# Performance work log

Measured on AMD Instinct MI355X. Metric: run time of the kernel, lower is better.

The kernel has to match this reference:

```python
import jax, jax.numpy as jnp
import numpy as np

B, L, D = 2, 2048, 2048
H, HKV, HD = 16, 4, 128
GROUPS = H // HKV


def _rope_tables(key):
    # standard RoPE cos/sin tables, shape (B, L, HD)
    inv_freq = 1.0 / (10000.0 ** (jnp.arange(0, HD, 2, dtype=jnp.float32) / HD))
    pos = jnp.arange(L, dtype=jnp.float32)
    freqs = pos[:, None] * inv_freq[None, :]          # (L, HD/2)
    emb = jnp.concatenate([freqs, freqs], axis=-1)    # (L, HD)
    cos = jnp.broadcast_to(jnp.cos(emb)[None], (B, L, HD))
    sin = jnp.broadcast_to(jnp.sin(emb)[None], (B, L, HD))
    return cos, sin


def setup_inputs() -> dict:
    key = jax.random.key(0)
    ks = jax.random.split(key, 5)
    x = jax.random.normal(ks[0], (B, L, D), dtype=jnp.float32)
    cos, sin = _rope_tables(ks[1])
    s = 1.0 / np.sqrt(D)
    Wq = jax.random.normal(ks[2], (D, D), dtype=jnp.float32) * s
    bq = jnp.zeros((D,), dtype=jnp.float32)
    Wkv = jax.random.normal(ks[3], (2 * HKV * HD, D), dtype=jnp.float32) * s
    bkv = jnp.zeros((2 * HKV * HD,), dtype=jnp.float32)
    Wo = jax.random.normal(ks[4], (D, D), dtype=jnp.float32) * s
    bo = jnp.zeros((D,), dtype=jnp.float32)
    return {"x": x, "cos": cos, "sin": sin, "Wq": Wq, "bq": bq,
            "Wkv": Wkv, "bkv": bkv, "Wo": Wo, "bo": bo}


def _rotate_half(t):
    t1, t2 = jnp.split(t, 2, axis=-1)
    return jnp.concatenate([-t2, t1], axis=-1)


def reference(x, cos, sin, Wq, bq, Wkv, bkv, Wo, bo):
    b, l, d = x.shape
    # QKV projections
    q = (x @ Wq.T + bq).reshape(b, l, H, HD)
    kv = (x @ Wkv.T + bkv).reshape(b, l, 2, HKV, HD)
    k, v = kv[:, :, 0], kv[:, :, 1]
    # RoPE (unsqueeze over head dim, layout B,L,H,D)
    c = cos[:, :, None, :]
    s = sin[:, :, None, :]
    q = q * c + _rotate_half(q) * s
    k = k * c + _rotate_half(k) * s
    # GQA: expand kv heads to query heads
    k = jnp.repeat(k, GROUPS, axis=2)
    v = jnp.repeat(v, GROUPS, axis=2)
    # causal attention (flash_attn_func equivalent math)
    scores = jnp.einsum("blhd,bmhd->bhlm", q, k) / jnp.sqrt(jnp.float32(HD))
    mask = jnp.tril(jnp.ones((l, l), dtype=bool))
    scores = jnp.where(mask[None, None], scores, jnp.finfo(scores.dtype).min)
    attn = jax.nn.softmax(scores, axis=-1)
    out = jnp.einsum("bhlm,bmhd->blhd", attn, v).reshape(b, l, H * HD)
    return out @ Wo.T + bo
```

## Files before the change

kernel.cpp:

```cpp
#include <hip/hip_runtime.h>
#include <hip/hip_bf16.h>
#include <cstddef>

constexpr int B = 2, L = 2048, D = 2048;
constexpr int H = 16, HKV = 4, HD = 128;
constexpr int GROUPS = H / HKV;
constexpr int KVD = 2 * HKV * HD;
constexpr int M_ROWS = B * L;
constexpr int QKVW = D + KVD;

typedef __attribute__((ext_vector_type(8))) short short8;
typedef __attribute__((ext_vector_type(4))) short s16x4;
typedef __attribute__((ext_vector_type(4))) float f32x4;

__device__ __forceinline__ short f2bf(float f) {
    union { float f; unsigned u; } v; v.f = f;
    unsigned r = v.u + 0x7FFFu + ((v.u >> 16) & 1u);
    return (short)(r >> 16);
}

__device__ __forceinline__ float fast_exp2(float x) {
#if __has_builtin(__builtin_amdgcn_exp2f)
    return __builtin_amdgcn_exp2f(x);
#else
    return exp2f(x);
#endif
}

__device__ __forceinline__ int invp(int pos) {
    const int b16 = pos >> 4, j = pos & 15;
    return ((b16 >> 1) << 4) + j + ((b16 & 1) << 6);
}

typedef __attribute__((address_space(1))) const void cg_void;
typedef __attribute__((address_space(3))) void lds_void;
__device__ __forceinline__ void gl_lds16(const void* g, void* l) {
    __builtin_amdgcn_global_load_lds((cg_void*)g, (lds_void*)l, 16, 0, 0);
}

__global__ __launch_bounds__(256) void cast_all(
    const float* __restrict__ x, const float* __restrict__ Wq,
    const float* __restrict__ Wkv, const float* __restrict__ Wo,
    const float* __restrict__ bq, const float* __restrict__ bkv,
    short* __restrict__ xb, short* __restrict__ wqkvb, short* __restrict__ wob,
    float* __restrict__ bqkv)
{
    constexpr int n_x   = M_ROWS * D / 4;
    constexpr int n_wq  = D * D / 4;
    constexpr int n_wkv = KVD * D / 4;
    constexpr int n_wo  = D * D / 4;
    constexpr int n_w   = n_x + n_wq + n_wkv + n_wo;
    constexpr int RPW   = D / 4;
    int i = blockIdx.x * 256 + threadIdx.x;
    if (i >= n_w) {
        const int j = i - n_w;
        float4 o;
#pragma unroll
        for (int e = 0; e < 4; ++e) {
            const int idx = j * 4 + e;
            float v;
            if (idx < D)                 v = bq[((idx >> 7) << 7) + invp(idx & 127)];
            else if (idx < D + HKV * HD) v = bkv[(((idx - D) >> 7) << 7) + invp((idx - D) & 127)];
            else                         v = bkv[idx - D];
            (&o.x)[e] = v;
        }
        ((float4*)bqkv)[j] = o;
        return;
    }
    const float* src; short* dst; int isrc;
    if (i < n_x) {
        src = x; dst = xb; isrc = i;
    } else if (i < n_x + n_wq) {
        i -= n_x; src = Wq; dst = wqkvb;
        const int fi = i / RPW, col = i % RPW;
        const int head = fi >> 7, pos = fi & 127;
        isrc = ((head << 7) + invp(pos)) * RPW + col;
    } else if (i < n_x + n_wq + n_wkv) {
        i -= n_x + n_wq; src = Wkv; dst = wqkvb + (size_t)D * D;
        const int fi = i / RPW, col = i % RPW;
        if (fi < HKV * HD) {
            isrc = (((fi >> 7) << 7) + invp(fi & 127)) * RPW + col;
        } else {
            isrc = i;
        }
    } else {
        i -= n_x + n_wq + n_wkv; src = Wo; dst = wob; isrc = i;
    }
    const float4 f = ((const float4*)src)[isrc];
    s16x4 s;
    s[0] = f2bf(f.x); s[1] = f2bf(f.y); s[2] = f2bf(f.z); s[3] = f2bf(f.w);
    ((s16x4*)dst)[i] = s;
}

template<int MODE>
__global__ __launch_bounds__(512, 2) void gemm256(
    const short* __restrict__ Ag, const short* __restrict__ Wg,
    const float* __restrict__ bias, float* __restrict__ C,
    const float* __restrict__ cosp, const float* __restrict__ sinp,
    short* __restrict__ qout, short* __restrict__ kout, short* __restrict__ vtout,
    int M, int N, int K)
{
    __shared__ __align__(1024) char smem[131072];

    const int tid = threadIdx.x;
    const int w = tid >> 6, lane = tid & 63;
    const int quad = lane >> 4, n16 = lane & 15;
    const int wr = w >> 2, wc = w & 3;

    const int nbx = gridDim.x;
    const int nwg = nbx * gridDim.y;
    int wg = blockIdx.y * nbx + blockIdx.x;
    wg = (wg & 7) * (nwg >> 3) + (wg >> 3);
    const int bm = (wg / nbx) << 8;
    const int bn = (wg % nbx) << 8;

    const int nkt = K >> 6;

    const int sbo = n16 * 64 + ((quad * 16) ^ ((n16 & 8) << 2));

    const int srow = lane >> 2;
    const int scol = ((lane & 3) * 8) ^ (((lane >> 5) & 1) << 4);

    f32x4 acc[8][4];
#pragma unroll
    for (int i = 0; i < 8; ++i)
#pragma unroll
        for (int j = 0; j < 4; ++j)
#pragma unroll
            for (int r = 0; r < 4; ++r) acc[i][j][r] = 0.f;

    short8 afr[4][2], bfr[4][2];

#define STAGE_A(k0, cb, h)                                                     \
    { _Pragma("unroll") for (int j = 0; j < 2; ++j) {                          \
        const int s  = w + j * 8;                                              \
        const int u  = s >> 1;                                                 \
        const int rg = ((u >> 2) << 3) + ((h) << 2) + (u & 3);                 \
        const int gr = bm + (rg << 4) + srow;                                  \
        const int gc = (k0) + ((s & 1) << 5) + scol;                           \
        gl_lds16(Ag + (size_t)gr * K + gc,                                     \
                 smem + (cb) * 32768 + (h) * 16384 + (s << 10)); } }

#define STAGE_B(k0, cb, h)                                                     \
    { _Pragma("unroll") for (int j = 0; j < 2; ++j) {                          \
        const int s  = w + j * 8;                                              \
        const int u  = s >> 1;                                                 \
        const int rg = ((u >> 1) << 2) + ((h) << 1) + (u & 1);                 \
        const int gr = bn + (rg << 4) + srow;                                  \
        const int gc = (k0) + ((s & 1) << 5) + scol;                           \
        gl_lds16(Wg + (size_t)gr * K + gc,                                     \
                 smem + 65536 + (cb) * 32768 + (h) * 16384 + (s << 10)); } }

#define PHASE(CB, MH, RDB, STAGE_STMT, WAIT_STMT)                              \
    {                                                                          \
        if (RDB) {                                                             \
            _Pragma("unroll") for (int nj = 0; nj < 4; ++nj)                   \
            _Pragma("unroll") for (int kk = 0; kk < 2; ++kk)                   \
                bfr[nj][kk] = *(const short8*)(smem + 65536 + (CB) * 32768 +   \
                    (nj >> 1) * 16384 +                                        \
                    ((((wc * 2 + (nj & 1)) * 2) + kk) << 10) + sbo);           \
        }                                                                      \
        _Pragma("unroll") for (int mi2 = 0; mi2 < 4; ++mi2)                    \
        _Pragma("unroll") for (int kk = 0; kk < 2; ++kk)                       \
            afr[mi2][kk] = *(const short8*)(smem + (CB) * 32768 +              \
                (MH) * 16384 + ((((wr * 4 + mi2) * 2) + kk) << 10) + sbo);     \
        STAGE_STMT;                                                            \
        WAIT_STMT;                                                             \
        __builtin_amdgcn_s_barrier();                                          \
        asm volatile("s_waitcnt lgkmcnt(0)" ::: "memory");                     \
        __builtin_amdgcn_sched_barrier(0);                                     \
        __builtin_amdgcn_s_setprio(1);                                         \
        _Pragma("unroll") for (int mi2 = 0; mi2 < 4; ++mi2)                    \
        _Pragma("unroll") for (int nj = 0; nj < 4; ++nj)                       \
        _Pragma("unroll") for (int kk = 0; kk < 2; ++kk)                       \
            acc[(MH) * 4 + mi2][nj] =                                          \
                __builtin_amdgcn_mfma_f32_16x16x32_bf16(                       \
                    afr[mi2][kk], bfr[nj][kk], acc[(MH) * 4 + mi2][nj],        \
                    0, 0, 0);                                                  \
        __builtin_amdgcn_s_setprio(0);                                         \
        asm volatile("" ::: "memory");                                         \
        __builtin_amdgcn_s_barrier();                                          \
    }

#define NOP_WAIT asm volatile("" ::: "memory")

    STAGE_A(0, 0, 0);
    STAGE_B(0, 0, 0);
    STAGE_A(0, 0, 1);
    STAGE_B(0, 0, 1);
    if (nkt > 1) {
        STAGE_A(64, 1, 0);
        STAGE_B(64, 1, 0);
        asm volatile("s_waitcnt vmcnt(4)" ::: "memory");
    } else {
        asm volatile("s_waitcnt vmcnt(0)" ::: "memory");
    }
    __builtin_amdgcn_s_barrier();

    for (int t = 0; t < nkt; t += 2) {
        const int k1 = (t + 1) << 6, k2 = (t + 2) << 6, k3 = (t + 3) << 6;
        const bool g2 = (t + 2) < nkt, g3 = (t + 3) < nkt;

        PHASE(0, 0, 1, { STAGE_A(k1, 1, 1); STAGE_B(k1, 1, 1); }, NOP_WAIT);
        PHASE(0, 1, 0, { if (g2) { STAGE_A(k2, 0, 0); STAGE_B(k2, 0, 0); } },
              { if (g2) asm volatile("s_waitcnt vmcnt(4)" ::: "memory");
                else    asm volatile("s_waitcnt vmcnt(0)" ::: "memory"); });

        PHASE(1, 0, 1, { if (g2) { STAGE_A(k2, 0, 1); STAGE_B(k2, 0, 1); } }, NOP_WAIT);
        PHASE(1, 1, 0, { if (g3) { STAGE_A(k3, 1, 0); STAGE_B(k3, 1, 0); } },
              { if (g3) asm volatile("s_waitcnt vmcnt(4)" ::: "memory");
                else    asm volatile("s_waitcnt vmcnt(0)" ::: "memory"); });
    }

#undef PHASE
#undef STAGE_A
#undef STAGE_B
#undef NOP_WAIT

    if (MODE == 0) {
#pragma unroll
        for (int mh = 0; mh < 2; ++mh)
#pragma unroll
            for (int mi2 = 0; mi2 < 4; ++mi2)
#pragma unroll
                for (int r = 0; r < 4; ++r) {
                    const int row = bm + wr * 128 + mh * 64 + mi2 * 16 + quad * 4 + r;
#pragma unroll
                    for (int nh = 0; nh < 2; ++nh)
#pragma unroll
                        for (int ni2 = 0; ni2 < 2; ++ni2) {
                            const int col = bn + wc * 64 + nh * 32 + ni2 * 16 + n16;
                            C[(size_t)row * N + col] =
                                acc[mh * 4 + mi2][nh * 2 + ni2][r] + bias[col];
                        }
                }
    } else {
        short* const T = (short*)smem;
        __syncthreads();
        if (bn < D + HKV * HD) {
#pragma unroll
            for (int mh = 0; mh < 2; ++mh)
#pragma unroll
                for (int mi2 = 0; mi2 < 4; ++mi2)
#pragma unroll
                    for (int r = 0; r < 4; ++r) {
                        const int rl = wr * 128 + mh * 64 + mi2 * 16 + quad * 4 + r;
                        const int row = bm + rl;
                        const float* csrow = cosp + (size_t)row * HD;
                        const float* snrow = sinp + (size_t)row * HD;
                        const int sw = ((rl >> 2) & 7) << 4;
#pragma unroll
                        for (int nh = 0; nh < 2; ++nh) {
                            const int cl = wc * 64 + nh * 32 + n16;
                            const int iif = (wc & 1) * 32 + nh * 16 + n16;
                            const float a  = acc[mh * 4 + mi2][nh * 2 + 0][r] + bias[bn + cl];
                            const float bb = acc[mh * 4 + mi2][nh * 2 + 1][r] + bias[bn + cl + 16];
                            const float olo = a * csrow[iif]       - bb * snrow[iif];
                            const float ohi = bb * csrow[iif + 64] + a * snrow[iif + 64];
                            *(short*)((char*)T + ((rl * 512 + cl * 2) ^ sw))        = f2bf(olo);
                            *(short*)((char*)T + ((rl * 512 + (cl + 16) * 2) ^ sw)) = f2bf(ohi);
                        }
                    }
            __syncthreads();
            const bool isK = (bn >= D);
#pragma unroll
            for (int it = 0; it < 16; ++it) {
                const int idx = it * 512 + tid;
                const int rl = idx >> 5, c8 = idx & 31;
                const short8 v = *(const short8*)((char*)T +
                    ((rl * 512 + c8 * 16) ^ (((rl >> 2) & 7) << 4)));
                const int row = bm + rl;
                if (!isK) {
                    *(short8*)&qout[(size_t)row * D + bn + c8 * 8] = v;
                } else {
                    const int ck = bn - D + c8 * 8;
                    const int hk = ck >> 7, dk = ck & 127;
                    const int b_ = row >> 11, l_ = row & (L - 1);
                    *(short8*)&kout[((size_t)(b_ * HKV + hk) * L + l_) * HD + dk] = v;
                }
            }
        } else {
#pragma unroll
            for (int mh = 0; mh < 2; ++mh)
#pragma unroll
                for (int mi2 = 0; mi2 < 4; ++mi2) {
                    const int l0 = wr * 128 + mh * 64 + mi2 * 16 + quad * 4;
#pragma unroll
                    for (int nh = 0; nh < 2; ++nh)
#pragma unroll
                        for (int ni2 = 0; ni2 < 2; ++ni2) {
                            const int cl = wc * 64 + nh * 32 + ni2 * 16 + n16;
                            const float bs = bias[bn + cl];
                            s16x4 sv;
#pragma unroll
                            for (int r = 0; r < 4; ++r)
                                sv[r] = f2bf(acc[mh * 4 + mi2][nh * 2 + ni2][r] + bs);
                            *(s16x4*)((char*)T + ((cl * 512 + l0 * 2) ^ ((cl & 7) << 4))) = sv;
                        }
                }
            __syncthreads();
#pragma unroll
            for (int it = 0; it < 16; ++it) {
                const int idx = it * 512 + tid;
                const int cvr = idx >> 5, l8 = idx & 31;
                const short8 v = *(const short8*)((char*)T +
                    ((cvr * 512 + l8 * 16) ^ ((cvr & 7) << 4)));
                const int cv = bn - (D + HKV * HD) + cvr;
                const int hv = cv >> 7, dv = cv & 127;
                const int b_ = bm >> 11;
                const int lg = (bm & (L - 1)) + l8 * 8;
                *(short8*)&vtout[((size_t)(b_ * HKV + hv) * HD + dv) * L + lg] = v;
            }
        }
    }
}

__global__ __launch_bounds__(512, 2) void gemm_out(
    const short* __restrict__ Ag, const short* __restrict__ Wg,
    const float* __restrict__ bias, float* __restrict__ C,
    int M, int N, int K)
{
    __shared__ __align__(1024) char smem[98304];

    const int tid = threadIdx.x;
    const int w = tid >> 6, lane = tid & 63;
    const int quad = lane >> 4, n16 = lane & 15;
    const int wr = w >> 2, wc = w & 3;

    const int nbx = gridDim.x;
    const int nwg = nbx * gridDim.y;
    int wg = blockIdx.y * nbx + blockIdx.x;
    wg = (wg & 7) * (nwg >> 3) + (wg >> 3);
    const int bm = (wg / nbx) << 7;
    const int bn = (wg % nbx) << 8;

    const int nkt = K >> 6;

    const int sbo = n16 * 64 + ((quad * 16) ^ ((n16 & 8) << 2));
    const int srow = lane >> 2;
    const int scol = ((lane & 3) * 8) ^ (((lane >> 5) & 1) << 4);

    f32x4 acc[4][4];
#pragma unroll
    for (int i = 0; i < 4; ++i)
#pragma unroll
        for (int j = 0; j < 4; ++j)
#pragma unroll
            for (int r = 0; r < 4; ++r) acc[i][j][r] = 0.f;

    short8 afr[4], bfr[4];

#define OSTAGE_A(k0, cb, kh)                                                   \
    { const int gr = bm + (w << 4) + srow;                                     \
      const int gc = (k0) + ((kh) << 5) + scol;                                \
      gl_lds16(Ag + (size_t)gr * K + gc,                                       \
               smem + (cb) * 16384 + (kh) * 8192 + (w << 10)); }

#define OSTAGE_B(k0, cb, kh)                                                   \
    { _Pragma("unroll") for (int j = 0; j < 2; ++j) {                          \
        const int s = w + j * 8;                                               \
        const int gr = bn + (s << 4) + srow;                                   \
        const int gc = (k0) + ((kh) << 5) + scol;                              \
        gl_lds16(Wg + (size_t)gr * K + gc,                                     \
                 smem + 32768 + (cb) * 32768 + (kh) * 16384 + (s << 10)); } }

#define OPHASE(CB, KH, STAGE_STMT, WAIT_STMT)                                  \
    {                                                                          \
        _Pragma("unroll") for (int mi = 0; mi < 4; ++mi)                       \
            afr[mi] = *(const short8*)(smem + (CB) * 16384 + (KH) * 8192 +     \
                ((wr * 4 + mi) << 10) + sbo);                                  \
        _Pragma("unroll") for (int nj = 0; nj < 4; ++nj)                       \
            bfr[nj] = *(const short8*)(smem + 32768 + (CB) * 32768 +           \
                (KH) * 16384 + ((wc * 4 + nj) << 10) + sbo);                   \
        STAGE_STMT;                                                            \
        WAIT_STMT;                                                             \
        __builtin_amdgcn_s_barrier();                                          \
        asm volatile("s_waitcnt lgkmcnt(0)" ::: "memory");                     \
        __builtin_amdgcn_sched_barrier(0);                                     \
        __builtin_amdgcn_s_setprio(1);                                         \
        _Pragma("unroll") for (int mi = 0; mi < 4; ++mi)                       \
        _Pragma("unroll") for (int nj = 0; nj < 4; ++nj)                       \
            acc[mi][nj] = __builtin_amdgcn_mfma_f32_16x16x32_bf16(             \
                afr[mi], bfr[nj], acc[mi][nj], 0, 0, 0);                       \
        __builtin_amdgcn_s_setprio(0);                                         \
        asm volatile("" ::: "memory");                                         \
        __builtin_amdgcn_s_barrier();                                          \
    }

#define ONOP asm volatile("" ::: "memory")

    OSTAGE_A(0, 0, 0);
    OSTAGE_B(0, 0, 0);
    OSTAGE_A(0, 0, 1);
    OSTAGE_B(0, 0, 1);
    if (nkt > 1) {
        OSTAGE_A(64, 1, 0);
        OSTAGE_B(64, 1, 0);
        asm volatile("s_waitcnt vmcnt(3)" ::: "memory");
    } else {
        asm volatile("s_waitcnt vmcnt(0)" ::: "memory");
    }
    __builtin_amdgcn_s_barrier();

    for (int t = 0; t < nkt; t += 2) {
        const int k1 = (t + 1) << 6, k2 = (t + 2) << 6, k3 = (t + 3) << 6;
        const bool g2 = (t + 2) < nkt, g3 = (t + 3) < nkt;

        OPHASE(0, 0, { OSTAGE_A(k1, 1, 1); OSTAGE_B(k1, 1, 1); }, ONOP);
        OPHASE(0, 1, { if (g2) { OSTAGE_A(k2, 0, 0); OSTAGE_B(k2, 0, 0); } },
               { if (g2) asm volatile("s_waitcnt vmcnt(3)" ::: "memory");
                 else    asm volatile("s_waitcnt vmcnt(0)" ::: "memory"); });

        OPHASE(1, 0, { if (g2) { OSTAGE_A(k2, 0, 1); OSTAGE_B(k2, 0, 1); } }, ONOP);
        OPHASE(1, 1, { if (g3) { OSTAGE_A(k3, 1, 0); OSTAGE_B(k3, 1, 0); } },
               { if (g3) asm volatile("s_waitcnt vmcnt(3)" ::: "memory");
                 else    asm volatile("s_waitcnt vmcnt(0)" ::: "memory"); });
    }

#undef OPHASE
#undef OSTAGE_A
#undef OSTAGE_B
#undef ONOP

#pragma unroll
    for (int mi = 0; mi < 4; ++mi)
#pragma unroll
        for (int r = 0; r < 4; ++r) {
            const int row = bm + wr * 64 + mi * 16 + quad * 4 + r;
#pragma unroll
            for (int nj = 0; nj < 4; ++nj) {
                const int col = bn + wc * 64 + nj * 16 + n16;
                C[(size_t)row * N + col] = acc[mi][nj][r] + bias[col];
            }
        }
}

__global__ __launch_bounds__(512, 4) void attn_mfma5(
    const short* __restrict__ qb_, const short* __restrict__ kb_,
    const short* __restrict__ vtb_, short* __restrict__ ob)
{
    __shared__ __align__(16) char smem[75776];
    short* const KsB  = (short*)smem;
    short* const VtB  = (short*)(smem + 32768);
    short* const PbB  = (short*)(smem + 65536);
    float* const Rbuf = (float*)smem;

    const int hkv = blockIdx.y, b = blockIdx.z;
    const int tid = threadIdx.x;
    const int w = tid >> 6, lane = tid & 63;
    const int quad = lane >> 4, n16 = lane & 15;
    const int h   = hkv * GROUPS + (w & 3);
    const int kh  = (w >> 2) * 32;
    const int khg = (w >> 2) * 4;

    const size_t kbase  = (size_t)(b * HKV + hkv) * L * HD;
    const size_t vtbase = (size_t)(b * HKV + hkv) * HD * L;
    const float c1 = 0.12751845f;
    const float c0 = -28.853901f;

    short8 ones;
#pragma unroll
    for (int i = 0; i < 8; ++i) ones[i] = (short)0x3F80;

    const int kr = lane >> 4;
    const int kg_sw = lane & 15;
    const int vr = lane >> 3;
    const int vg_sw = lane & 7;

    short* const myPb = PbB + w * (16 * 40);

#pragma unroll 1
    for (int phase = 0; phase < 2; ++phase) {
        const int qidx = phase ? (127 - (int)blockIdx.x) : (int)blockIdx.x;
        const int qb0 = qidx * 16;
        const int ntiles = (qidx >> 2) + 1;

        short8 qf[4];
#pragma unroll
        for (int kk = 0; kk < 4; ++kk)
            qf[kk] = *(const short8*)&qb_[
                ((size_t)(b * L + qb0 + n16)) * D + h * HD + kk * 32 + quad * 8];

        f32x4 oacc[8], lacc;
#pragma unroll
        for (int r = 0; r < 4; ++r) lacc[r] = 0.f;
#pragma unroll
        for (int nt = 0; nt < 8; ++nt)
#pragma unroll
            for (int r = 0; r < 4; ++r) oacc[nt][r] = 0.f;

        __syncthreads();

        {
            const short* kg = kb_ + kbase;
            const short* vg = vtb_ + vtbase;
#pragma unroll
            for (int j = 0; j < 2; ++j) {
                const int chunk = w * 2 + j;
                const int r = chunk * 4 + kr;
                gl_lds16(kg + r * HD + (kg_sw ^ (r & 15)) * 8, KsB + chunk * 512);
            }
#pragma unroll
            for (int j = 0; j < 2; ++j) {
                const int chunk = w * 2 + j;
                const int d = chunk * 8 + vr;
                gl_lds16(vg + (size_t)d * L + (vg_sw ^ (d & 7)) * 8, VtB + chunk * 512);
            }
        }

        for (int kt = 0; kt < ntiles; ++kt) {
            const int buf = kt & 1;
            __syncthreads();

            if (kt + 1 < ntiles) {
                const short* kg = kb_ + kbase + (size_t)((kt + 1) * 64) * HD;
                const short* vg = vtb_ + vtbase + (kt + 1) * 64;
#pragma unroll
                for (int j = 0; j < 2; ++j) {
                    const int chunk = w * 2 + j;
                    const int r = chunk * 4 + kr;
                    gl_lds16(kg + r * HD + (kg_sw ^ (r & 15)) * 8,
                             KsB + (buf ^ 1) * 8192 + chunk * 512);
                }
#pragma unroll
                for (int j = 0; j < 2; ++j) {
                    const int chunk = w * 2 + j;
                    const int d = chunk * 8 + vr;
                    gl_lds16(vg + (size_t)d * L + (vg_sw ^ (d & 7)) * 8,
                             VtB + (buf ^ 1) * 8192 + chunk * 512);
                }
            }

            const short* Ks = KsB + buf * 8192;
            const short* Vt = VtB + buf * 8192;

            f32x4 s[2];
#pragma unroll
            for (int ktl = 0; ktl < 2; ++ktl)
#pragma unroll
                for (int r = 0; r < 4; ++r) s[ktl][r] = 0.f;
            __builtin_amdgcn_s_setprio(1);
#pragma unroll
            for (int kk = 0; kk < 4; ++kk) {
                short8 kf[2];
#pragma unroll
                for (int ktl = 0; ktl < 2; ++ktl) {
                    const int row = kh + ktl * 16 + n16;
                    kf[ktl] = *(const short8*)&Ks[row * 128 + ((kk * 4 + quad) ^ n16) * 8];
                }
#pragma unroll
                for (int ktl = 0; ktl < 2; ++ktl)
                    s[ktl] = __builtin_amdgcn_mfma_f32_16x16x32_bf16(
                        qf[kk], kf[ktl], s[ktl], 0, 0, 0);
            }
            __builtin_amdgcn_s_setprio(0);

            const bool lastt = (kt == ntiles - 1);
#pragma unroll
            for (int ktl = 0; ktl < 2; ++ktl) {
                const int key0 = kt * 64 + kh + ktl * 16 + n16;
#pragma unroll
                for (int r = 0; r < 4; ++r) {
                    float sv = s[ktl][r];
                    if (lastt) {
                        const int qi = qb0 + quad * 4 + r;
                        sv = (key0 <= qi) ? sv : -1e30f;
                    }
                    const float e = fast_exp2(sv * c1 + c0);
                    myPb[(quad * 4 + r) * 40 + ktl * 16 + n16] = f2bf(e);
                }
            }
            asm volatile("s_waitcnt lgkmcnt(0)" ::: "memory");

            const short8 pf = *(const short8*)&myPb[n16 * 40 + quad * 8];
            __builtin_amdgcn_s_setprio(1);
            lacc = __builtin_amdgcn_mfma_f32_16x16x32_bf16(pf, ones, lacc, 0, 0, 0);
#pragma unroll
            for (int nt = 0; nt < 8; ++nt) {
                const short8 vf = *(const short8*)&Vt[
                    (nt * 16 + n16) * 64 + ((khg + quad) ^ (n16 & 7)) * 8];
                oacc[nt] = __builtin_amdgcn_mfma_f32_16x16x32_bf16(pf, vf, oacc[nt], 0, 0, 0);
            }
            __builtin_amdgcn_s_setprio(0);
        }

        __syncthreads();
        if (w >= 4) {
            float* rp = Rbuf + ((size_t)(w - 4) * 64 + lane) * 40;
#pragma unroll
            for (int nt = 0; nt < 8; ++nt)
                *(f32x4*)&rp[nt * 4] = oacc[nt];
            *(f32x4*)&rp[32] = lacc;
        }
        __syncthreads();
        if (w < 4) {
            const float* rp = Rbuf + ((size_t)w * 64 + lane) * 40;
            const f32x4 lr = *(const f32x4*)&rp[32];
#pragma unroll
            for (int r = 0; r < 4; ++r) lacc[r] += lr[r];
#pragma unroll
            for (int nt = 0; nt < 8; ++nt) {
                const f32x4 o2 = *(const f32x4*)&rp[nt * 4];
#pragma unroll
                for (int r = 0; r < 4; ++r) oacc[nt][r] += o2[r];
            }
#pragma unroll
            for (int r = 0; r < 4; ++r) {
                const float inv = 1.0f / lacc[r];
                short* op = ob + ((size_t)(b * L + qb0 + quad * 4 + r)) * D + h * HD + n16;
#pragma unroll
                for (int nt = 0; nt < 8; ++nt) op[nt * 16] = f2bf(oacc[nt][r] * inv);
            }
        }
    }
}

extern "C" void kernel_launch(void* const* d_in, const int* in_sizes, int n_in,
                              void* d_out, int out_size, void* d_ws, size_t ws_size,
                              hipStream_t stream)
{
    const float* x    = (const float*)d_in[0];
    const float* cosp = (const float*)d_in[1];
    const float* sinp = (const float*)d_in[2];
    const float* Wq   = (const float*)d_in[3];
    const float* bq   = (const float*)d_in[4];
    const float* Wkv  = (const float*)d_in[5];
    const float* bkv  = (const float*)d_in[6];
    const float* Wo   = (const float*)d_in[7];
    const float* bo   = (const float*)d_in[8];
    float* out = (float*)d_out;

    char* p = (char*)d_ws;
    short* x_bf    = (short*)p; p += (size_t)M_ROWS * D * 2;
    short* wqkv_bf = (short*)p; p += (size_t)QKVW * D * 2;
    short* wo_bf   = (short*)p; p += (size_t)D * D * 2;
    float* b_qkv   = (float*)p; p += (size_t)QKVW * 4;
    short* q_bf    = (short*)p; p += (size_t)M_ROWS * D * 2;
    short* k_bf    = (short*)p; p += (size_t)M_ROWS * HKV * HD * 2;
    short* vt_bf   = (short*)p;
    short* attn_bf = x_bf;

    dim3 blk(256);

    cast_all<<<dim3(18435), blk, 0, stream>>>(
        x, Wq, Wkv, Wo, bq, bkv, x_bf, wqkv_bf, wo_bf, b_qkv);

    gemm256<1><<<dim3(QKVW / 256, M_ROWS / 256), dim3(512), 0, stream>>>(
        x_bf, wqkv_bf, b_qkv, nullptr, cosp, sinp, q_bf, k_bf, vt_bf,
        M_ROWS, QKVW, D);

    attn_mfma5<<<dim3(64, HKV, B), dim3(512), 0, stream>>>(q_bf, k_bf, vt_bf, attn_bf);

    gemm_out<<<dim3(D / 256, M_ROWS / 128), dim3(512), 0, stream>>>(
        attn_bf, wo_bf, bo, out, M_ROWS, D, D);
}
```

Baseline: 281.5 us.

## Replace pipelined 256-tile GEMMs with a simple 128-tile single-buffer GEMM

Swaps the software-pipelined, double-buffered 256x256 QKV GEMM and the 128x256 output GEMM for one simpler 128x128 tile kernel with 256 threads and a K step of 32. That kernel loads each stage synchronously and uses two __syncthreads per K step. The RoPE and V-transpose epilogues are adapted to the smaller tile, and the output projection now uses the same kernel in MODE 0. The apparent aim is more workgroups and higher occupancy from less LDS per block, at the cost of losing the copy/compute overlap and the larger per-block data reuse.

Result: slower. 322.9 us (+14.7%).

```diff
diff --git a/kernel.cpp b/kernel.cpp
--- a/kernel.cpp
+++ b/kernel.cpp
@@ -93,218 +93,145 @@
 }
 
 template<int MODE>
-__global__ __launch_bounds__(512, 2) void gemm256(
+__global__ __launch_bounds__(256) void gemm128(
     const short* __restrict__ Ag, const short* __restrict__ Wg,
     const float* __restrict__ bias, float* __restrict__ C,
     const float* __restrict__ cosp, const float* __restrict__ sinp,
     short* __restrict__ qout, short* __restrict__ kout, short* __restrict__ vtout,
     int M, int N, int K)
 {
-    __shared__ __align__(1024) char smem[131072];
+    __shared__ __align__(1024) char smem[32768];
+    short* const As = (short*)smem;
+    short* const Bs = (short*)(smem + 8192);
 
     const int tid = threadIdx.x;
     const int w = tid >> 6, lane = tid & 63;
     const int quad = lane >> 4, n16 = lane & 15;
-    const int wr = w >> 2, wc = w & 3;
+    const int wm = (w & 1) * 64, wn = (w >> 1) * 64;
 
     const int nbx = gridDim.x;
     const int nwg = nbx * gridDim.y;
     int wg = blockIdx.y * nbx + blockIdx.x;
     wg = (wg & 7) * (nwg >> 3) + (wg >> 3);
-    const int bm = (wg / nbx) << 8;
-    const int bn = (wg % nbx) << 8;
-
-    const int nkt = K >> 6;
-
-    const int sbo = n16 * 64 + ((quad * 16) ^ ((n16 & 8) << 2));
-
-    const int srow = lane >> 2;
-    const int scol = ((lane & 3) * 8) ^ (((lane >> 5) & 1) << 4);
-
-    f32x4 acc[8][4];
-#pragma unroll
-    for (int i = 0; i < 8; ++i)
+    const int bm = (wg / nbx) << 7;
+    const int bn = (wg % nbx) << 7;
+
+    const int sr = lane >> 2;
+    const int sc = (((lane & 3) ^ ((lane >> 3) & 3)) * 8);
+
+    const int rsw = ((n16 >> 1) & 3);
+
+    f32x4 acc[4][4];
+#pragma unroll
+    for (int i = 0; i < 4; ++i)
 #pragma unroll
         for (int j = 0; j < 4; ++j)
 #pragma unroll
             for (int r = 0; r < 4; ++r) acc[i][j][r] = 0.f;
 
-    short8 afr[4][2], bfr[4][2];
-
-#define STAGE_A(k0, cb, h)                                                     \
-    { _Pragma("unroll") for (int j = 0; j < 2; ++j) {                          \
-        const int s  = w + j * 8;                                              \
-        const int u  = s >> 1;                                                 \
-        const int rg = ((u >> 2) << 3) + ((h) << 2) + (u & 3);                 \
-        const int gr = bm + (rg << 4) + srow;                                  \
-        const int gc = (k0) + ((s & 1) << 5) + scol;                           \
-        gl_lds16(Ag + (size_t)gr * K + gc,                                     \
-                 smem + (cb) * 32768 + (h) * 16384 + (s << 10)); } }
-
-#define STAGE_B(k0, cb, h)                                                     \
-    { _Pragma("unroll") for (int j = 0; j < 2; ++j) {                          \
-        const int s  = w + j * 8;                                              \
-        const int u  = s >> 1;                                                 \
-        const int rg = ((u >> 1) << 2) + ((h) << 1) + (u & 1);                 \
-        const int gr = bn + (rg << 4) + srow;                                  \
-        const int gc = (k0) + ((s & 1) << 5) + scol;                           \
-        gl_lds16(Wg + (size_t)gr * K + gc,                                     \
-                 smem + 65536 + (cb) * 32768 + (h) * 16384 + (s << 10)); } }
-
-#define PHASE(CB, MH, RDB, STAGE_STMT, WAIT_STMT)                              \
-    {                                                                          \
-        if (RDB) {                                                             \
-            _Pragma("unroll") for (int nj = 0; nj < 4; ++nj)                   \
-            _Pragma("unroll") for (int kk = 0; kk < 2; ++kk)                   \
-                bfr[nj][kk] = *(const short8*)(smem + 65536 + (CB) * 32768 +   \
-                    (nj >> 1) * 16384 +                                        \
-                    ((((wc * 2 + (nj & 1)) * 2) + kk) << 10) + sbo);           \
-        }                                                                      \
-        _Pragma("unroll") for (int mi2 = 0; mi2 < 4; ++mi2)                    \
-        _Pragma("unroll") for (int kk = 0; kk < 2; ++kk)                       \
-            afr[mi2][kk] = *(const short8*)(smem + (CB) * 32768 +              \
-                (MH) * 16384 + ((((wr * 4 + mi2) * 2) + kk) << 10) + sbo);     \
-        STAGE_STMT;                                                            \
-        WAIT_STMT;                                                             \
-        __builtin_amdgcn_s_barrier();                                          \
-        asm volatile("s_waitcnt lgkmcnt(0)" ::: "memory");                     \
-        __builtin_amdgcn_sched_barrier(0);                                     \
-        __builtin_amdgcn_s_setprio(1);                                         \
-        _Pragma("unroll") for (int mi2 = 0; mi2 < 4; ++mi2)                    \
-        _Pragma("unroll") for (int nj = 0; nj < 4; ++nj)                       \
-        _Pragma("unroll") for (int kk = 0; kk < 2; ++kk)                       \
-            acc[(MH) * 4 + mi2][nj] =                                          \
-                __builtin_amdgcn_mfma_f32_16x16x32_bf16(                       \
-                    afr[mi2][kk], bfr[nj][kk], acc[(MH) * 4 + mi2][nj],        \
-                    0, 0, 0);                                                  \
-        __builtin_amdgcn_s_setprio(0);                                         \
-        asm volatile("" ::: "memory");                                         \
-        __builtin_amdgcn_s_barrier();                                          \
+    for (int k0 = 0; k0 < K; k0 += 32) {
+#pragma unroll
+        for (int it = 0; it < 2; ++it) {
+            const int row0 = it * 64 + w * 16;
+            gl_lds16(Ag + (size_t)(bm + row0 + sr) * K + k0 + sc, &As[row0 * 32]);
+            gl_lds16(Wg + (size_t)(bn + row0 + sr) * K + k0 + sc, &Bs[row0 * 32]);
+        }
+        __syncthreads();
+
+        short8 af[4], bf[4];
+#pragma unroll
+        for (int mt = 0; mt < 4; ++mt)
+            af[mt] = *(const short8*)&As[(wm + mt * 16 + n16) * 32 + ((quad ^ rsw) * 8)];
+#pragma unroll
+        for (int nt = 0; nt < 4; ++nt)
+            bf[nt] = *(const short8*)&Bs[(wn + nt * 16 + n16) * 32 + ((quad ^ rsw) * 8)];
+        __builtin_amdgcn_s_setprio(1);
+#pragma unroll
+        for (int mt = 0; mt < 4; ++mt)
+#pragma unroll
+            for (int nt = 0; nt < 4; ++nt)
+                acc[mt][nt] = __builtin_amdgcn_mfma_f32_16x16x32_bf16(
+                    af[mt], bf[nt], acc[mt][nt], 0, 0, 0);
+        __builtin_amdgcn_s_setprio(0);
+        __syncthreads();
     }
 
-#define NOP_WAIT asm volatile("" ::: "memory")
-
-    STAGE_A(0, 0, 0);
-    STAGE_B(0, 0, 0);
-    STAGE_A(0, 0, 1);
-    STAGE_B(0, 0, 1);
-    if (nkt > 1) {
-        STAGE_A(64, 1, 0);
-        STAGE_B(64, 1, 0);
-        asm volatile("s_waitcnt vmcnt(4)" ::: "memory");
-    } else {
-        asm volatile("s_waitcnt vmcnt(0)" ::: "memory");
-    }
-    __builtin_amdgcn_s_barrier();
-
-    for (int t = 0; t < nkt; t += 2) {
-        const int k1 = (t + 1) << 6, k2 = (t + 2) << 6, k3 = (t + 3) << 6;
-        const bool g2 = (t + 2) < nkt, g3 = (t + 3) < nkt;
-
-        PHASE(0, 0, 1, { STAGE_A(k1, 1, 1); STAGE_B(k1, 1, 1); }, NOP_WAIT);
-        PHASE(0, 1, 0, { if (g2) { STAGE_A(k2, 0, 0); STAGE_B(k2, 0, 0); } },
-              { if (g2) asm volatile("s_waitcnt vmcnt(4)" ::: "memory");
-                else    asm volatile("s_waitcnt vmcnt(0)" ::: "memory"); });
-
-        PHASE(1, 0, 1, { if (g2) { STAGE_A(k2, 0, 1); STAGE_B(k2, 0, 1); } }, NOP_WAIT);
-        PHASE(1, 1, 0, { if (g3) { STAGE_A(k3, 1, 0); STAGE_B(k3, 1, 0); } },
-              { if (g3) asm volatile("s_waitcnt vmcnt(4)" ::: "memory");
-                else    asm volatile("s_waitcnt vmcnt(0)" ::: "memory"); });
-    }
-
-#undef PHASE
-#undef STAGE_A
-#undef STAGE_B
-#undef NOP_WAIT
-
     if (MODE == 0) {
 #pragma unroll
-        for (int mh = 0; mh < 2; ++mh)
-#pragma unroll
-            for (int mi2 = 0; mi2 < 4; ++mi2)
-#pragma unroll
-                for (int r = 0; r < 4; ++r) {
-                    const int row = bm + wr * 128 + mh * 64 + mi2 * 16 + quad * 4 + r;
-#pragma unroll
-                    for (int nh = 0; nh < 2; ++nh)
-#pragma unroll
-                        for (int ni2 = 0; ni2 < 2; ++ni2) {
-                            const int col = bn + wc * 64 + nh * 32 + ni2 * 16 + n16;
-                            C[(size_t)row * N + col] =
-                                acc[mh * 4 + mi2][nh * 2 + ni2][r] + bias[col];
-                        }
-                }
+        for (int mt = 0; mt < 4; ++mt)
+#pragma unroll
+            for (int r = 0; r < 4; ++r) {
+                const int row = bm + wm + mt * 16 + quad * 4 + r;
+#pragma unroll
+                for (int nt = 0; nt < 4; ++nt) {
+                    const int col = bn + wn + nt * 16 + n16;
+                    C[(size_t)row * N + col] = acc[mt][nt][r] + bias[col];
+                }
+            }
     } else {
         short* const T = (short*)smem;
         __syncthreads();
         if (bn < D + HKV * HD) {
 #pragma unroll
-            for (int mh = 0; mh < 2; ++mh)
-#pragma unroll
-                for (int mi2 = 0; mi2 < 4; ++mi2)
-#pragma unroll
-                    for (int r = 0; r < 4; ++r) {
-                        const int rl = wr * 128 + mh * 64 + mi2 * 16 + quad * 4 + r;
-                        const int row = bm + rl;
-                        const float* csrow = cosp + (size_t)row * HD;
-                        const float* snrow = sinp + (size_t)row * HD;
-                        const int sw = ((rl >> 2) & 7) << 4;
-#pragma unroll
-                        for (int nh = 0; nh < 2; ++nh) {
-                            const int cl = wc * 64 + nh * 32 + n16;
-                            const int iif = (wc & 1) * 32 + nh * 16 + n16;
-                            const float a  = acc[mh * 4 + mi2][nh * 2 + 0][r] + bias[bn + cl];
-                            const float bb = acc[mh * 4 + mi2][nh * 2 + 1][r] + bias[bn + cl + 16];
-                            const float olo = a * csrow[iif]       - bb * snrow[iif];
-                            const float ohi = bb * csrow[iif + 64] + a * snrow[iif + 64];
-                            *(short*)((char*)T + ((rl * 512 + cl * 2) ^ sw))        = f2bf(olo);
-                            *(short*)((char*)T + ((rl * 512 + (cl + 16) * 2) ^ sw)) = f2bf(ohi);
-                        }
+            for (int mt = 0; mt < 4; ++mt)
+#pragma unroll
+                for (int r = 0; r < 4; ++r) {
+                    const int rl = wm + mt * 16 + quad * 4 + r;
+                    const int row = bm + rl;
+                    const float* csrow = cosp + (size_t)row * HD;
+                    const float* snrow = sinp + (size_t)row * HD;
+                    const int sw = ((rl >> 2) & 7) << 4;
+#pragma unroll
+                    for (int ntp = 0; ntp < 2; ++ntp) {
+                        const int cl = wn + ntp * 32 + n16;
+                        const int iif = n16 + (wn >> 1) + ntp * 16;
+                        const float a  = acc[mt][2 * ntp + 0][r] + bias[bn + cl];
+                        const float bb = acc[mt][2 * ntp + 1][r] + bias[bn + cl + 16];
+                        const float olo = a * csrow[iif]       - bb * snrow[iif];
+                        const float ohi = bb * csrow[iif + 64] + a * snrow[iif + 64];
+                        *(short*)((char*)T + ((rl * 256 + cl * 2) ^ sw))        = f2bf(olo);
+                        *(short*)((char*)T + ((rl * 256 + (cl + 16) * 2) ^ sw)) = f2bf(ohi);
                     }
+                }
             __syncthreads();
             const bool isK = (bn >= D);
 #pragma unroll
-            for (int it = 0; it < 16; ++it) {
-                const int idx = it * 512 + tid;
-                const int rl = idx >> 5, c8 = idx & 31;
+            for (int it = 0; it < 8; ++it) {
+                const int idx = it * 256 + tid;
+                const int rl = idx >> 4, c8 = idx & 15;
                 const short8 v = *(const short8*)((char*)T +
-                    ((rl * 512 + c8 * 16) ^ (((rl >> 2) & 7) << 4)));
+                    ((rl * 256 + c8 * 16) ^ (((rl >> 2) & 7) << 4)));
                 const int row = bm + rl;
                 if (!isK) {
                     *(short8*)&qout[(size_t)row * D + bn + c8 * 8] = v;
                 } else {
-                    const int ck = bn - D + c8 * 8;
-                    const int hk = ck >> 7, dk = ck & 127;
+                    const int hk = (bn - D) >> 7;
                     const int b_ = row >> 11, l_ = row & (L - 1);
-                    *(short8*)&kout[((size_t)(b_ * HKV + hk) * L + l_) * HD + dk] = v;
+                    *(short8*)&kout[((size_t)(b_ * HKV + hk) * L + l_) * HD + c8 * 8] = v;
                 }
             }
         } else {
 #pragma unroll
-            for (int mh = 0; mh < 2; ++mh)
-#pragma unroll
-                for (int mi2 = 0; mi2 < 4; ++mi2) {
-                    const int l0 = wr * 128 + mh * 64 + mi2 * 16 + quad * 4;
-#pragma unroll
-                    for (int nh = 0; nh < 2; ++nh)
-#pragma unroll
-                        for (int ni2 = 0; ni2 < 2; ++ni2) {
-                            const int cl = wc * 64 + nh * 32 + ni2 * 16 + n16;
-                            const float bs = bias[bn + cl];
-                            s16x4 sv;
-#pragma unroll
-                            for (int r = 0; r < 4; ++r)
-                                sv[r] = f2bf(acc[mh * 4 + mi2][nh * 2 + ni2][r] + bs);
-                            *(s16x4*)((char*)T + ((cl * 512 + l0 * 2) ^ ((cl & 7) << 4))) = sv;
-                        }
-                }
+            for (int mt = 0; mt < 4; ++mt) {
+                const int l0 = wm + mt * 16 + quad * 4;
+#pragma unroll
+                for (int nt = 0; nt < 4; ++nt) {
+                    const int cl = wn + nt * 16 + n16;
+                    const float bs = bias[bn + cl];
+                    s16x4 sv;
+#pragma unroll
+                    for (int r = 0; r < 4; ++r)
+                        sv[r] = f2bf(acc[mt][nt][r] + bs);
+                    *(s16x4*)((char*)T + ((cl * 256 + l0 * 2) ^ ((cl & 7) << 4))) = sv;
+                }
+            }
             __syncthreads();
 #pragma unroll
-            for (int it = 0; it < 16; ++it) {
-                const int idx = it * 512 + tid;
-                const int cvr = idx >> 5, l8 = idx & 31;
+            for (int it = 0; it < 8; ++it) {
+                const int idx = it * 256 + tid;
+                const int cvr = idx >> 4, l8 = idx & 15;
                 const short8 v = *(const short8*)((char*)T +
-                    ((cvr * 512 + l8 * 16) ^ ((cvr & 7) << 4)));
+                    ((cvr * 256 + l8 * 16) ^ ((cvr & 7) << 4)));
                 const int cv = bn - (D + HKV * HD) + cvr;
                 const int hv = cv >> 7, dv = cv & 127;
                 const int b_ = bm >> 11;
@@ -313,126 +240,6 @@
             }
         }
     }
-}
-
-__global__ __launch_bounds__(512, 2) void gemm_out(
-    const short* __restrict__ Ag, const short* __restrict__ Wg,
-    const float* __restrict__ bias, float* __restrict__ C,
-    int M, int N, int K)
-{
-    __shared__ __align__(1024) char smem[98304];
-
-    const int tid = threadIdx.x;
-    const int w = tid >> 6, lane = tid & 63;
-    const int quad = lane >> 4, n16 = lane & 15;
-    const int wr = w >> 2, wc = w & 3;
-
-    const int nbx = gridDim.x;
-    const int nwg = nbx * gridDim.y;
-    int wg = blockIdx.y * nbx + blockIdx.x;
-    wg = (wg & 7) * (nwg >> 3) + (wg >> 3);
-    const int bm = (wg / nbx) << 7;
-    const int bn = (wg % nbx) << 8;
-
-    const int nkt = K >> 6;
-
-    const int sbo = n16 * 64 + ((quad * 16) ^ ((n16 & 8) << 2));
-    const int srow = lane >> 2;
-    const int scol = ((lane & 3) * 8) ^ (((lane >> 5) & 1) << 4);
-
-    f32x4 acc[4][4];
-#pragma unroll
-    for (int i = 0; i < 4; ++i)
-#pragma unroll
-        for (int j = 0; j < 4; ++j)
-#pragma unroll
-            for (int r = 0; r < 4; ++r) acc[i][j][r] = 0.f;
-
-    short8 afr[4], bfr[4];
-
-#define OSTAGE_A(k0, cb, kh)                                                   \
-    { const int gr = bm + (w << 4) + srow;                                     \
-      const int gc = (k0) + ((kh) << 5) + scol;                                \
-      gl_lds16(Ag + (size_t)gr * K + gc,                                       \
-               smem + (cb) * 16384 + (kh) * 8192 + (w << 10)); }
-
-#define OSTAGE_B(k0, cb, kh)                                                   \
-    { _Pragma("unroll") for (int j = 0; j < 2; ++j) {                          \
-        const int s = w + j * 8;                                               \
-        const int gr = bn + (s << 4) + srow;                                   \
-        const int gc = (k0) + ((kh) << 5) + scol;                              \
-        gl_lds16(Wg + (size_t)gr * K + gc,                                     \
-                 smem + 32768 + (cb) * 32768 + (kh) * 16384 + (s << 10)); } }
-
-#define OPHASE(CB, KH, STAGE_STMT, WAIT_STMT)                                  \
-    {                                                                          \
-        _Pragma("unroll") for (int mi = 0; mi < 4; ++mi)                       \
-            afr[mi] = *(const short8*)(smem + (CB) * 16384 + (KH) * 8192 +     \
-                ((wr * 4 + mi) << 10) + sbo);                                  \
-        _Pragma("unroll") for (int nj = 0; nj < 4; ++nj)                       \
-            bfr[nj] = *(const short8*)(smem + 32768 + (CB) * 32768 +           \
-                (KH) * 16384 + ((wc * 4 + nj) << 10) + sbo);                   \
-        STAGE_STMT;                                                            \
-        WAIT_STMT;                                                             \
-        __builtin_amdgcn_s_barrier();                                          \
-        asm volatile("s_waitcnt lgkmcnt(0)" ::: "memory");                     \
-        __builtin_amdgcn_sched_barrier(0);                                     \
-        __builtin_amdgcn_s_setprio(1);                                         \
-        _Pragma("unroll") for (int mi = 0; mi < 4; ++mi)                       \
-        _Pragma("unroll") for (int nj = 0; nj < 4; ++nj)                       \
-            acc[mi][nj] = __builtin_amdgcn_mfma_f32_16x16x32_bf16(             \
-                afr[mi], bfr[nj], acc[mi][nj], 0, 0, 0);                       \
-        __builtin_amdgcn_s_setprio(0);                                         \
-        asm volatile("" ::: "memory");                                         \
-        __builtin_amdgcn_s_barrier();                                          \
-    }
-
-#define ONOP asm volatile("" ::: "memory")
-
-    OSTAGE_A(0, 0, 0);
-    OSTAGE_B(0, 0, 0);
-    OSTAGE_A(0, 0, 1);
-    OSTAGE_B(0, 0, 1);
-    if (nkt > 1) {
-        OSTAGE_A(64, 1, 0);
-        OSTAGE_B(64, 1, 0);
-        asm volatile("s_waitcnt vmcnt(3)" ::: "memory");
-    } else {
-        asm volatile("s_waitcnt vmcnt(0)" ::: "memory");
-    }
-    __builtin_amdgcn_s_barrier();
-
-    for (int t = 0; t < nkt; t += 2) {
-        const int k1 = (t + 1) << 6, k2 = (t + 2) << 6, k3 = (t + 3) << 6;
-        const bool g2 = (t + 2) < nkt, g3 = (t + 3) < nkt;
-
-        OPHASE(0, 0, { OSTAGE_A(k1, 1, 1); OSTAGE_B(k1, 1, 1); }, ONOP);
-        OPHASE(0, 1, { if (g2) { OSTAGE_A(k2, 0, 0); OSTAGE_B(k2, 0, 0); } },
-               { if (g2) asm volatile("s_waitcnt vmcnt(3)" ::: "memory");
-                 else    asm volatile("s_waitcnt vmcnt(0)" ::: "memory"); });
-
-        OPHASE(1, 0, { if (g2) { OSTAGE_A(k2, 0, 1); OSTAGE_B(k2, 0, 1); } }, ONOP);
-        OPHASE(1, 1, { if (g3) { OSTAGE_A(k3, 1, 0); OSTAGE_B(k3, 1, 0); } },
-               { if (g3) asm volatile("s_waitcnt vmcnt(3)" ::: "memory");
-                 else    asm volatile("s_waitcnt vmcnt(0)" ::: "memory"); });
-    }
-
-#undef OPHASE
-#undef OSTAGE_A
-#undef OSTAGE_B
-#undef ONOP
-
-#pragma unroll
-    for (int mi = 0; mi < 4; ++mi)
-#pragma unroll
-        for (int r = 0; r < 4; ++r) {
-            const int row = bm + wr * 64 + mi * 16 + quad * 4 + r;
-#pragma unroll
-            for (int nj = 0; nj < 4; ++nj) {
-                const int col = bn + wc * 64 + nj * 16 + n16;
-                C[(size_t)row * N + col] = acc[mi][nj][r] + bias[col];
-            }
-        }
 }
 
 __global__ __launch_bounds__(512, 4) void attn_mfma5(
@@ -645,12 +452,13 @@
     cast_all<<<dim3(18435), blk, 0, stream>>>(
         x, Wq, Wkv, Wo, bq, bkv, x_bf, wqkv_bf, wo_bf, b_qkv);
 
-    gemm256<1><<<dim3(QKVW / 256, M_ROWS / 256), dim3(512), 0, stream>>>(
+    gemm128<1><<<dim3(QKVW / 128, M_ROWS / 128), blk, 0, stream>>>(
         x_bf, wqkv_bf, b_qkv, nullptr, cosp, sinp, q_bf, k_bf, vt_bf,
         M_ROWS, QKVW, D);
 
     attn_mfma5<<<dim3(64, HKV, B), dim3(512), 0, stream>>>(q_bf, k_bf, vt_bf, attn_bf);
 
-    gemm_out<<<dim3(D / 256, M_ROWS / 128), dim3(512), 0, stream>>>(
-        attn_bf, wo_bf, bo, out, M_ROWS, D, D);
-}
+    gemm128<0><<<dim3(D / 128, M_ROWS / 128), blk, 0, stream>>>(
+        attn_bf, wo_bf, bo, out, nullptr, nullptr, nullptr, nullptr, nullptr,
+        M_ROWS, D, D);
+}
```
